# Kernel tuning notes

Measured on AMD Instinct MI355X. Metric: run time of the kernel, lower is better.

## Reference

```python
import jax, jax.numpy as jnp
import numpy as np

NB_CLUSTERS = 128   # C: number of clusters (equal-size, sorted ids)
PTS_PER_CLUSTER = 1024  # P: points per cluster
DIM = 3


def setup_inputs() -> dict:
    key = jax.random.key(0)
    k1, k2 = jax.random.split(key)
    n = NB_CLUSTERS * PTS_PER_CLUSTER
    input_points = jax.random.normal(k1, (n, DIM), dtype=jnp.float32)
    output_points = jax.random.normal(k2, (n, DIM), dtype=jnp.float32)
    clusters = jnp.repeat(jnp.arange(NB_CLUSTERS, dtype=jnp.int32), PTS_PER_CLUSTER)
    return {
        "input_points": input_points,
        "input_clusters": clusters,
        "output_points": output_points,
        "output_clusters": clusters,
    }


def reference(input_points, input_clusters, output_points, output_clusters):
    # Original: nb_clusters = max(input_clusters); loop for i in range(nb_clusters)
    # -> the HIGHEST cluster id is excluded from the loss. Reproduced via mask.
    nb = jnp.max(input_clusters)  # == NB_CLUSTERS - 1
    a = input_points.reshape(NB_CLUSTERS, PTS_PER_CLUSTER, DIM)   # [C,P,3]
    b = output_points.reshape(NB_CLUSTERS, PTS_PER_CLUSTER, DIM)  # [C,P,3]

    # Pairwise squared distances per cluster: d[c,i,j] = ||a[c,i]-b[c,j]||^2
    d = (jnp.sum(a * a, axis=-1)[:, :, None]
         + jnp.sum(b * b, axis=-1)[:, None, :]
         - 2.0 * jnp.einsum('cid,cjd->cij', a, b))  # [C,P,P]

    # Indices computed under no_grad in the original (ints: no grad anyway).
    idx1 = jnp.argmin(d, axis=2)  # for each input point: nearest output point
    idx2 = jnp.argmin(d, axis=1)  # for each output point: nearest input point

    near_b = jnp.take_along_axis(b, idx1[..., None], axis=1)  # [C,P,3]
    near_a = jnp.take_along_axis(a, idx2[..., None], axis=1)  # [C,P,3]

    l1 = jnp.sum((a - near_b) ** 2, axis=(1, 2))  # [C]
    l2 = jnp.sum((b - near_a) ** 2, axis=(1, 2))  # [C]

    mask = (jnp.arange(NB_CLUSTERS) < nb).astype(a.dtype)  # exclude last cluster
    return jnp.sum(mask * (l1 + l2))
```

## Files before the change

### kernel.cpp

```cpp
#include <hip/hip_runtime.h>


#define NB_CLUSTERS 128
#define PTS 1024
#define ACTIVE_CLUSTERS 127
#define Q 4
#define THREADS 256

__global__ __launch_bounds__(THREADS) void chamfer_kernel(
    const float* __restrict__ pts_in,
    const float* __restrict__ pts_out,
    float* __restrict__ out)
{
    const int c   = blockIdx.x >> 1;
    const int dir = blockIdx.x & 1;

    const float* __restrict__ query  = dir ? pts_out : pts_in;
    const float* __restrict__ target = dir ? pts_in  : pts_out;

    __shared__ __align__(16) float4 st[PTS];

    const int tid = threadIdx.x;
    const size_t base = (size_t)c * PTS * 3;

    #pragma unroll
    for (int k = 0; k < Q; ++k) {
        const int j = k * THREADS + tid;
        const float* tp = target + base + (size_t)j * 3;
        float x = tp[0], y = tp[1], z = tp[2];
        st[j] = make_float4(x, y, z, fmaf(x, x, fmaf(y, y, z * z)));
    }
    __syncthreads();

    float qx[Q], qy[Q], qz[Q], qn[Q], mn[Q];
    #pragma unroll
    for (int k = 0; k < Q; ++k) {
        const float* qp = query + base + (size_t)(k * THREADS + tid) * 3;
        float ax = qp[0], ay = qp[1], az = qp[2];
        qn[k] = fmaf(ax, ax, fmaf(ay, ay, az * az));
        qx[k] = -2.0f * ax;
        qy[k] = -2.0f * ay;
        qz[k] = -2.0f * az;
        mn[k] = 3.4e38f;
    }

    #pragma unroll 8
    for (int j = 0; j < PTS; ++j) {
        const float4 b = st[j];
        #pragma unroll
        for (int k = 0; k < Q; ++k) {
            float s = fmaf(qx[k], b.x, b.w);
            s = fmaf(qy[k], b.y, s);
            s = fmaf(qz[k], b.z, s);
            mn[k] = fminf(mn[k], s);
        }
    }

    float s = 0.0f;
    #pragma unroll
    for (int k = 0; k < Q; ++k) s += mn[k] + qn[k];

    #pragma unroll
    for (int off = 32; off > 0; off >>= 1)
        s += __shfl_down(s, off, 64);

    __shared__ float wsum[4];
    const int wave = tid >> 6;
    const int lane = tid & 63;
    if (lane == 0) wsum[wave] = s;
    __syncthreads();

    if (tid == 0) {
        float t = wsum[0] + wsum[1] + wsum[2] + wsum[3];
        atomicAdd(out, t);
    }
}

extern "C" void kernel_launch(void* const* d_in, const int* in_sizes, int n_in,
                              void* d_out, int out_size, void* d_ws, size_t ws_size,
                              hipStream_t stream) {
    const float* input_points  = (const float*)d_in[0];
    const float* output_points = (const float*)d_in[2];
    float* out = (float*)d_out;

    hipMemsetAsync(out, 0, sizeof(float), stream);

    chamfer_kernel<<<dim3(ACTIVE_CLUSTERS * 2), dim3(THREADS), 0, stream>>>(
        input_points, output_points, out);
}
```

Before: 95.53 us.

## Split target scan across 8 segments per block with shared-memory min reduction

Each block now uses 1024 threads: 128 query lanes times 8 target segments. Each thread holds 8 queries and scans only 128 targets. Partial minima are then combined through shared memory before the sum reduction. The aim is more waves per CU, since the earlier launch of 254 blocks of 256 threads gave low occupancy. The cost is an extra shared-memory reduction pass, more shared memory and register pressure per thread, and the loop body is unrolled to process two targets per iteration.

```diff
diff --git a/kernel.cpp b/kernel.cpp
--- a/kernel.cpp
+++ b/kernel.cpp
@@ -1,13 +1,15 @@
 #include <hip/hip_runtime.h>
 
 
-#define NB_CLUSTERS 128
 #define PTS 1024
 #define ACTIVE_CLUSTERS 127
-#define Q 4
-#define THREADS 256
+#define QG   128
+#define Q    8
+#define SEG  8
+#define TPB  1024
+#define TSEG (PTS / SEG)
 
-__global__ __launch_bounds__(THREADS) void chamfer_kernel(
+__global__ __launch_bounds__(TPB) void chamfer_kernel(
     const float* __restrict__ pts_in,
     const float* __restrict__ pts_out,
     float* __restrict__ out)
@@ -19,23 +21,23 @@
     const float* __restrict__ target = dir ? pts_in  : pts_out;
 
     __shared__ __align__(16) float4 st[PTS];
+    __shared__ float pm[SEG * Q * QG];
 
     const int tid = threadIdx.x;
+    const int qi  = tid & (QG - 1);
+    const int seg = tid >> 7;
     const size_t base = (size_t)c * PTS * 3;
 
-    #pragma unroll
-    for (int k = 0; k < Q; ++k) {
-        const int j = k * THREADS + tid;
-        const float* tp = target + base + (size_t)j * 3;
+    {
+        const float* tp = target + base + (size_t)tid * 3;
         float x = tp[0], y = tp[1], z = tp[2];
-        st[j] = make_float4(x, y, z, fmaf(x, x, fmaf(y, y, z * z)));
+        st[tid] = make_float4(x, y, z, fmaf(x, x, fmaf(y, y, z * z)));
     }
-    __syncthreads();
 
     float qx[Q], qy[Q], qz[Q], qn[Q], mn[Q];
     #pragma unroll
     for (int k = 0; k < Q; ++k) {
-        const float* qp = query + base + (size_t)(k * THREADS + tid) * 3;
+        const float* qp = query + base + (size_t)(k * QG + qi) * 3;
         float ax = qp[0], ay = qp[1], az = qp[2];
         qn[k] = fmaf(ax, ax, fmaf(ay, ay, az * az));
         qx[k] = -2.0f * ax;
@@ -43,36 +45,53 @@
         qz[k] = -2.0f * az;
         mn[k] = 3.4e38f;
     }
+    __syncthreads();
 
-    #pragma unroll 8
-    for (int j = 0; j < PTS; ++j) {
-        const float4 b = st[j];
+    const int j0 = seg * TSEG;
+    #pragma unroll 4
+    for (int jj = 0; jj < TSEG; jj += 2) {
+        const float4 b0 = st[j0 + jj];
+        const float4 b1 = st[j0 + jj + 1];
         #pragma unroll
         for (int k = 0; k < Q; ++k) {
-            float s = fmaf(qx[k], b.x, b.w);
-            s = fmaf(qy[k], b.y, s);
-            s = fmaf(qz[k], b.z, s);
-            mn[k] = fminf(mn[k], s);
+            float s0 = fmaf(qx[k], b0.x, b0.w);
+            s0 = fmaf(qy[k], b0.y, s0);
+            s0 = fmaf(qz[k], b0.z, s0);
+            float s1 = fmaf(qx[k], b1.x, b1.w);
+            s1 = fmaf(qy[k], b1.y, s1);
+            s1 = fmaf(qz[k], b1.z, s1);
+            mn[k] = fminf(fminf(s0, s1), mn[k]);
         }
     }
 
-    float s = 0.0f;
     #pragma unroll
-    for (int k = 0; k < Q; ++k) s += mn[k] + qn[k];
+    for (int k = 0; k < Q; ++k)
+        pm[(seg * Q + k) * QG + qi] = mn[k] + qn[k];
+    __syncthreads();
+
+    const int k2  = tid >> 7;
+    const int qi2 = tid & (QG - 1);
+    float v = 3.4e38f;
+    #pragma unroll
+    for (int s = 0; s < SEG; ++s)
+        v = fminf(v, pm[(s * Q + k2) * QG + qi2]);
 
     #pragma unroll
     for (int off = 32; off > 0; off >>= 1)
-        s += __shfl_down(s, off, 64);
+        v += __shfl_down(v, off, 64);
 
-    __shared__ float wsum[4];
+    __shared__ float wsum[16];
     const int wave = tid >> 6;
     const int lane = tid & 63;
-    if (lane == 0) wsum[wave] = s;
+    if (lane == 0) wsum[wave] = v;
     __syncthreads();
 
-    if (tid == 0) {
-        float t = wsum[0] + wsum[1] + wsum[2] + wsum[3];
-        atomicAdd(out, t);
+    if (wave == 0) {
+        float t = (lane < 16) ? wsum[lane] : 0.0f;
+        #pragma unroll
+        for (int off = 8; off > 0; off >>= 1)
+            t += __shfl_down(t, off, 64);
+        if (lane == 0) atomicAdd(out, t);
     }
 }
 
@@ -85,6 +104,6 @@
 
     hipMemsetAsync(out, 0, sizeof(float), stream);
 
-    chamfer_kernel<<<dim3(ACTIVE_CLUSTERS * 2), dim3(THREADS), 0, stream>>>(
+    chamfer_kernel<<<dim3(ACTIVE_CLUSTERS * 2), dim3(TPB), 0, stream>>>(
         input_points, output_points, out);
 }
```

After: 83.36 us. -12.7%, faster.
